# Optimization experiments

Hardware: AMD Instinct MI355X
Metric: run time of the kernel (lower is better)

Reference implementation:

```python
import jax, jax.numpy as jnp
import numpy as np

N, E = 50000, 800000
F_IN, HID, H, LBL = 512, 16, 8, 40
HC = HID * H  # 128
BN_EPS = 1e-5
ELU_ALPHA = 0.2
NEG_SLOPE = 0.2


def setup_inputs() -> dict:
    key = jax.random.key(0)
    ks = jax.random.split(key, 32)
    inp = {}
    inp['x'] = jax.random.normal(ks[0], (N, F_IN), dtype=jnp.float32)
    inp['edge_index'] = jax.random.randint(ks[1], (2, E), 0, N, dtype=jnp.int32)
    # layer 0: F_IN -> (H, HID), concat
    inp['W0'] = jax.random.normal(ks[2], (F_IN, HC), dtype=jnp.float32) * 0.05
    inp['as0'] = jax.random.normal(ks[3], (H, HID), dtype=jnp.float32) * 0.1
    inp['ad0'] = jax.random.normal(ks[4], (H, HID), dtype=jnp.float32) * 0.1
    inp['b0'] = jnp.zeros((HC,), jnp.float32)
    inp['g0'] = jnp.ones((HC,), jnp.float32)
    inp['be0'] = jnp.zeros((HC,), jnp.float32)
    inp['rm0'] = jnp.zeros((HC,), jnp.float32)
    inp['rv0'] = jnp.ones((HC,), jnp.float32)
    # layer 1: HC -> (H, HID), concat
    inp['W1'] = jax.random.normal(ks[5], (HC, HC), dtype=jnp.float32) * 0.1
    inp['as1'] = jax.random.normal(ks[6], (H, HID), dtype=jnp.float32) * 0.1
    inp['ad1'] = jax.random.normal(ks[7], (H, HID), dtype=jnp.float32) * 0.1
    inp['b1'] = jnp.zeros((HC,), jnp.float32)
    inp['g1'] = jnp.ones((HC,), jnp.float32)
    inp['be1'] = jnp.zeros((HC,), jnp.float32)
    inp['rm1'] = jnp.zeros((HC,), jnp.float32)
    inp['rv1'] = jnp.ones((HC,), jnp.float32)
    # layer 2: HC -> (1, LBL), mean (concat=False)
    inp['W2'] = jax.random.normal(ks[8], (HC, LBL), dtype=jnp.float32) * 0.1
    inp['as2'] = jax.random.normal(ks[9], (1, LBL), dtype=jnp.float32) * 0.1
    inp['ad2'] = jax.random.normal(ks[10], (1, LBL), dtype=jnp.float32) * 0.1
    inp['b2'] = jnp.zeros((LBL,), jnp.float32)
    return inp


def _gat_conv(xf, src, dst, W, a_src, a_dst, b, heads, out_ch, concat):
    # PyG GATConv (eval): linear -> per-head attn logits -> segment softmax over dst -> scatter-add
    n = xf.shape[0]
    h = (xf @ W).reshape(n, heads, out_ch)            # [N,H,C]
    alpha_s = jnp.einsum('nhc,hc->nh', h, a_src)      # [N,H]
    alpha_d = jnp.einsum('nhc,hc->nh', h, a_dst)
    e = jax.nn.leaky_relu(alpha_s[src] + alpha_d[dst], NEG_SLOPE)  # [Etot,H]
    m = jax.ops.segment_max(e, dst, num_segments=n)
    e = jnp.exp(e - m[dst])
    s = jax.ops.segment_sum(e, dst, num_segments=n)
    alpha = e / (s[dst] + 1e-16)                      # [Etot,H]
    msg = alpha[:, :, None] * h[src]                  # [Etot,H,C]
    out = jax.ops.segment_sum(msg, dst, num_segments=n)  # [N,H,C]
    out = out.reshape(n, heads * out_ch) if concat else out.mean(axis=1)
    return out + b


def _bn_elu(xf, g, be, rm, rv):
    y = (xf - rm) * (g * jax.lax.rsqrt(rv + BN_EPS)) + be
    return jnp.where(y > 0, y, ELU_ALPHA * jnp.expm1(y))


def reference(x, edge_index, W0, as0, ad0, b0, g0, be0, rm0, rv0,
              W1, as1, ad1, b1, g1, be1, rm1, rv1, W2, as2, ad2, b2):
    n = x.shape[0]
    # add self-loops (PyG GATConv default add_self_loops=True)
    loops = jnp.arange(n, dtype=edge_index.dtype)
    src = jnp.concatenate([edge_index[0], loops])
    dst = jnp.concatenate([edge_index[1], loops])
    h = _gat_conv(x, src, dst, W0, as0, ad0, b0, H, HID, True)
    h = _bn_elu(h, g0, be0, rm0, rv0)
    h = _gat_conv(h, src, dst, W1, as1, ad1, b1, H, HID, True)
    h = _bn_elu(h, g1, be1, rm1, rv1)
    out = _gat_conv(h, src, dst, W2, as2, ad2, b2, 1, LBL, False)
    return out
```

## Files before the change

### kernel.cpp

```cpp
#include <hip/hip_runtime.h>
#include <hip/hip_bf16.h>
#include <cstdint>
#include <cstddef>

#define NN 50000
#define EE 800000
#define FIN 512
#define HIDC 16
#define NH 8
#define HCH 128
#define NLBL 40
#define NLBLP 48
#define ETOT (EE + NN)
#define NEG_SLOPE 0.2f
#define ELU_A 0.2f
#define BN_EPS 1e-5f
#define SCH 8192
#define NCHK 7

typedef __attribute__((ext_vector_type(8))) short bf16x8;
typedef __attribute__((ext_vector_type(4))) short bf16x4;
typedef __attribute__((ext_vector_type(4))) float f32x4;

__device__ inline short f2b(float f) {
    __hip_bfloat16 h = __float2bfloat16(f);
    return *reinterpret_cast<short*>(&h);
}
__device__ inline float blo(unsigned int u) {
    union { unsigned int u; float f; } v; v.u = u << 16; return v.f;
}
__device__ inline float bhi(unsigned int u) {
    union { unsigned int u; float f; } v; v.u = u & 0xffff0000u; return v.f;
}

__global__ __launch_bounds__(256) void k_prep(const float* __restrict__ W0, short* __restrict__ Wt0,
                                              const float* __restrict__ W1, short* __restrict__ Wt1,
                                              const float* __restrict__ W2, short* __restrict__ Wt2,
                                              const int* __restrict__ ei, int* __restrict__ deg)
{
    int b = blockIdx.x;
    int tid = threadIdx.x;
    if (b < 256) {
        int idx = b * 256 + tid;
        int n = idx >> 9, k = idx & 511;
        Wt0[idx] = f2b(W0[(size_t)k * HCH + n]);
        return;
    }
    b -= 256;
    if (b < 64) {
        int idx = b * 256 + tid;
        int n = idx >> 7, k = idx & 127;
        Wt1[idx] = f2b(W1[(size_t)k * HCH + n]);
        return;
    }
    b -= 64;
    if (b < 24) {
        int idx = b * 256 + tid;
        int n = idx >> 7, k = idx & 127;
        Wt2[idx] = f2b(n < NLBL ? W2[(size_t)k * NLBL + n] : 0.f);
        return;
    }
    b -= 24;
    {
        int e = b * 256 + tid;
        if (e < ETOT) {
            int dst = (e < EE) ? ei[EE + e] : (e - EE);
            atomicAdd(&deg[dst], 1);
        }
    }
}

__global__ __launch_bounds__(1024) void k_scan1(const int* __restrict__ deg,
                                                int* __restrict__ row_ptr,
                                                int* __restrict__ tot)
{
    __shared__ int sm[1024];
    int b = blockIdx.x, tid = threadIdx.x;
    int i0 = b * SCH + tid * 8;
    int v[8];
    int s = 0;
    #pragma unroll
    for (int j = 0; j < 8; ++j) {
        int i = i0 + j;
        v[j] = (i < NN) ? deg[i] : 0;
        s += v[j];
    }
    sm[tid] = s;
    __syncthreads();
    for (int ofs = 1; ofs < 1024; ofs <<= 1) {
        int t = (tid >= ofs) ? sm[tid - ofs] : 0;
        __syncthreads();
        sm[tid] += t;
        __syncthreads();
    }
    int excl = sm[tid] - s;
    #pragma unroll
    for (int j = 0; j < 8; ++j) {
        int i = i0 + j;
        if (i < NN) row_ptr[i] = excl;
        excl += v[j];
    }
    if (tid == 1023) tot[b] = sm[1023];
}

__global__ __launch_bounds__(64) void k_scan2(const int* __restrict__ tot,
                                              int* __restrict__ totp,
                                              int* __restrict__ row_ptr)
{
    if (threadIdx.x == 0) {
        int run = 0;
        for (int i = 0; i < NCHK; ++i) { totp[i] = run; run += tot[i]; }
        row_ptr[NN] = run;
    }
}

__global__ __launch_bounds__(256) void k_scan3(int* __restrict__ row_ptr,
                                               int* __restrict__ cursor,
                                               const int* __restrict__ totp)
{
    int i = blockIdx.x * 256 + threadIdx.x;
    if (i < NN) {
        int v = row_ptr[i] + totp[i / SCH];
        row_ptr[i] = v;
        cursor[i] = v;
    }
}

__global__ __launch_bounds__(256) void k_scatter(const int* __restrict__ ei,
                                                 int* __restrict__ cursor,
                                                 int* __restrict__ csr_src)
{
    int e = blockIdx.x * blockDim.x + threadIdx.x;
    if (e >= ETOT) return;
    int src, dst;
    if (e < EE) { src = ei[e]; dst = ei[EE + e]; }
    else        { src = dst = e - EE; }
    int pos = atomicAdd(&cursor[dst], 1);
    csr_src[pos] = src;
}

template<int KDIM, bool A_BF16>
__global__ __launch_bounds__(512, 4) void k_gemm2(const void* __restrict__ Ap,
                                                  const short* __restrict__ Wt,
                                                  short* __restrict__ C,
                                                  int M,
                                                  const float* __restrict__ a_s,
                                                  const float* __restrict__ a_d,
                                                  float* __restrict__ as_o,
                                                  float* __restrict__ ad_o)
{
    constexpr int KCH  = 128;
    constexpr int NCH  = KDIM / KCH;
    constexpr int LROW = KCH + 8;
    __shared__ short As[64 * LROW];
    __shared__ short Bs[128 * LROW];

    const int tid  = threadIdx.x;
    const int wv   = tid >> 6;
    const int lane = tid & 63;
    const int quad = lane >> 4;
    const int col  = lane & 15;
    const int wr   = wv >> 1;
    const int wn   = wv & 1;
    const int rowbase = blockIdx.x * 64;

    const float* Af = (const float*)Ap;
    const short* Ab = (const short*)Ap;

    float4 pa[4];
    bf16x8 pab[2];
    bf16x8 pb[4];

    auto loadA = [&](int c) {
        if constexpr (A_BF16) {
            #pragma unroll
            for (int r = 0; r < 2; ++r) {
                int gr = rowbase + r * 32 + (tid >> 4);
                gr = gr < M ? gr : M - 1;
                pab[r] = *(const bf16x8*)(Ab + (size_t)gr * KDIM + c * KCH + (tid & 15) * 8);
            }
        } else {
            #pragma unroll
            for (int r = 0; r < 4; ++r) {
                int gr = rowbase + r * 16 + (tid >> 5);
                gr = gr < M ? gr : M - 1;
                pa[r] = *(const float4*)(Af + (size_t)gr * KDIM + c * KCH + (tid & 31) * 4);
            }
        }
    };
    auto loadB = [&](int c) {
        #pragma unroll
        for (int r = 0; r < 4; ++r) {
            int n = r * 32 + (tid >> 4);
            pb[r] = *(const bf16x8*)(Wt + (size_t)n * KDIM + c * KCH + (tid & 15) * 8);
        }
    };
    auto writeAB = [&]() {
        if constexpr (A_BF16) {
            #pragma unroll
            for (int r = 0; r < 2; ++r) {
                int row = r * 32 + (tid >> 4);
                *(bf16x8*)(As + row * LROW + (tid & 15) * 8) = pab[r];
            }
        } else {
            #pragma unroll
            for (int r = 0; r < 4; ++r) {
                int row = r * 16 + (tid >> 5);
                bf16x4 w;
                w[0] = f2b(pa[r].x); w[1] = f2b(pa[r].y);
                w[2] = f2b(pa[r].z); w[3] = f2b(pa[r].w);
                *(bf16x4*)(As + row * LROW + (tid & 31) * 4) = w;
            }
        }
        #pragma unroll
        for (int r = 0; r < 4; ++r) {
            int n = r * 32 + (tid >> 4);
            *(bf16x8*)(Bs + n * LROW + (tid & 15) * 8) = pb[r];
        }
    };

    f32x4 acc[4];
    #pragma unroll
    for (int t = 0; t < 4; ++t) acc[t] = (f32x4){0.f, 0.f, 0.f, 0.f};

    loadA(0); loadB(0);

    for (int c = 0; c < NCH; ++c) {
        writeAB();
        __syncthreads();
        if (c + 1 < NCH) { loadA(c + 1); loadB(c + 1); }
        #pragma unroll
        for (int s = 0; s < KCH / 32; ++s) {
            bf16x8 af = *(const bf16x8*)(As + (wr * 16 + col) * LROW + s * 32 + quad * 8);
            #pragma unroll
            for (int t = 0; t < 4; ++t) {
                bf16x8 bf = *(const bf16x8*)(Bs + (wn * 64 + t * 16 + col) * LROW + s * 32 + quad * 8);
                acc[t] = __builtin_amdgcn_mfma_f32_16x16x32_bf16(af, bf, acc[t], 0, 0, 0);
            }
        }
        if (c + 1 < NCH) __syncthreads();
    }

    const int mb = rowbase + wr * 16 + quad * 4;

    #pragma unroll
    for (int t = 0; t < 4; ++t) {
        int cc = wn * 64 + t * 16 + col;
        #pragma unroll
        for (int r = 0; r < 4; ++r) {
            int m = mb + r;
            if (m < M) C[(size_t)m * HCH + cc] = f2b(acc[t][r]);
        }
    }

    #pragma unroll
    for (int t = 0; t < 4; ++t) {
        int hh = wn * 4 + t;
        float ws = a_s[hh * HIDC + col];
        float wd = a_d[hh * HIDC + col];
        #pragma unroll
        for (int r = 0; r < 4; ++r) {
            float vs = acc[t][r] * ws;
            float vd = acc[t][r] * wd;
            vs += __shfl_xor(vs, 1);  vd += __shfl_xor(vd, 1);
            vs += __shfl_xor(vs, 2);  vd += __shfl_xor(vd, 2);
            vs += __shfl_xor(vs, 4);  vd += __shfl_xor(vd, 4);
            vs += __shfl_xor(vs, 8);  vd += __shfl_xor(vd, 8);
            int m = mb + r;
            if (col == 0 && m < M) {
                as_o[m * NH + hh] = vs;
                ad_o[m * NH + hh] = vd;
            }
        }
    }
}

template<int KDIM, int NTILES, bool A_BF16>
__global__ __launch_bounds__(256) void k_gemm_lds(const void* __restrict__ Ap,
                                                  const short* __restrict__ Wt,
                                                  short* __restrict__ C,
                                                  int M, int N,
                                                  const float* __restrict__ a_s2,
                                                  const float* __restrict__ a_d2,
                                                  float* __restrict__ as_o,
                                                  float* __restrict__ ad_o)
{
    constexpr int NFULL = NTILES * 16;
    constexpr int KCH = 128;
    constexpr int NK = KDIM / 32;
    constexpr int NCH = KDIM / KCH;
    constexpr int LROW = KCH + 8;
    __shared__ short Bs[NFULL * LROW];

    const int tid  = threadIdx.x;
    const int wave = tid >> 6;
    const int lane = tid & 63;
    const int quad = lane >> 4;
    const int col  = lane & 15;
    const int row  = blockIdx.x * 64 + wave * 16 + col;
    const int arow = row < M ? row : M - 1;

    f32x4 acc[NTILES];
    #pragma unroll
    for (int t = 0; t < NTILES; ++t) acc[t] = (f32x4){0.f, 0.f, 0.f, 0.f};

    bf16x8 arB[4];
    float4 arF[4][2];
    const short* Ab = (const short*)Ap;
    const float* Af = (const float*)Ap;
    auto pf = [&](int ks) {
        if (ks >= NK) return;
        if (A_BF16) {
            arB[ks & 3] = *(const bf16x8*)(Ab + (size_t)arow * KDIM + ks * 32 + quad * 8);
        } else {
            const float4* p = (const float4*)(Af + (size_t)arow * KDIM + ks * 32 + quad * 8);
            arF[ks & 3][0] = p[0];
            arF[ks & 3][1] = p[1];
        }
    };
    pf(0); pf(1); pf(2); pf(3);

    for (int c = 0; c < NCH; ++c) {
        const int k0 = c * KCH;
        constexpr int TOT8 = NFULL * (KCH / 8);
        #pragma unroll
        for (int i = tid; i < TOT8; i += 256) {
            int n  = i >> 4;
            int kk = i & 15;
            bf16x8 v = *(const bf16x8*)(Wt + (size_t)n * KDIM + k0 + kk * 8);
            *(bf16x8*)(Bs + n * LROW + kk * 8) = v;
        }
        __syncthreads();
        #pragma unroll
        for (int s = 0; s < KCH / 32; ++s) {
            const int ks = c * (KCH / 32) + s;
            bf16x8 afrag;
            if (A_BF16) {
                afrag = arB[ks & 3];
            } else {
                float4 v0 = arF[ks & 3][0], v1 = arF[ks & 3][1];
                afrag[0] = f2b(v0.x); afrag[1] = f2b(v0.y);
                afrag[2] = f2b(v0.z); afrag[3] = f2b(v0.w);
                afrag[4] = f2b(v1.x); afrag[5] = f2b(v1.y);
                afrag[6] = f2b(v1.z); afrag[7] = f2b(v1.w);
            }
            pf(ks + 4);
            #pragma unroll
            for (int t = 0; t < NTILES; ++t) {
                bf16x8 bfrag = *(const bf16x8*)(Bs + (t * 16 + col) * LROW + s * 32 + quad * 8);
                acc[t] = __builtin_amdgcn_mfma_f32_16x16x32_bf16(afrag, bfrag, acc[t], 0, 0, 0);
            }
        }
        if (c + 1 < NCH) __syncthreads();
    }

    const int mbase = blockIdx.x * 64 + wave * 16 + quad * 4;
    #pragma unroll
    for (int t = 0; t < NTILES; ++t) {
        int cc = t * 16 + col;
        if (cc < N) {
            #pragma unroll
            for (int r = 0; r < 4; ++r) {
                int m = mbase + r;
                if (m < M) C[(size_t)m * N + cc] = f2b(acc[t][r]);
            }
        }
    }

    float vs[4] = {0.f, 0.f, 0.f, 0.f};
    float vd[4] = {0.f, 0.f, 0.f, 0.f};
    #pragma unroll
    for (int t = 0; t < NTILES; ++t) {
        int cc = t * 16 + col;
        float ws = cc < NLBL ? a_s2[cc] : 0.f;
        float wd = cc < NLBL ? a_d2[cc] : 0.f;
        #pragma unroll
        for (int r = 0; r < 4; ++r) {
            vs[r] += acc[t][r] * ws;
            vd[r] += acc[t][r] * wd;
        }
    }
    #pragma unroll
    for (int r = 0; r < 4; ++r) {
        float s = vs[r], d = vd[r];
        s += __shfl_xor(s, 1);  d += __shfl_xor(d, 1);
        s += __shfl_xor(s, 2);  d += __shfl_xor(d, 2);
        s += __shfl_xor(s, 4);  d += __shfl_xor(d, 4);
        s += __shfl_xor(s, 8);  d += __shfl_xor(d, 8);
        int m = mbase + r;
        if (col == 0 && m < M) {
            as_o[m] = s;
            ad_o[m] = d;
        }
    }
}

__global__ __launch_bounds__(256) void k_agg(const int* __restrict__ row_ptr,
                                             const int* __restrict__ csr_src,
                                             const unsigned short* __restrict__ h,
                                             const float* __restrict__ as,
                                             const float* __restrict__ ad,
                                             const float* __restrict__ b,
                                             const float* __restrict__ g,
                                             const float* __restrict__ be,
                                             const float* __restrict__ rm,
                                             const float* __restrict__ rv,
                                             short* __restrict__ out)
{
    int n = blockIdx.x * 4 + (threadIdx.x >> 6);
    if (n >= NN) return;
    int lane = threadIdx.x & 63;
    int half = lane >> 5;
    int c4 = lane & 31;
    int hh = c4 >> 2;
    float adv = ad[n * NH + hh];
    float a0 = 0.f, a1 = 0.f, a2 = 0.f, a3 = 0.f, sw = 0.f;
    int jb = row_ptr[n], je = row_ptr[n + 1];
    int j = jb + half;
    for (; j + 6 < je; j += 8) {
        int s0 = csr_src[j];
        int s1 = csr_src[j + 2];
        int s2 = csr_src[j + 4];
        int s3 = csr_src[j + 6];
        float l0 = as[s0 * NH + hh] + adv;
        float l1 = as[s1 * NH + hh] + adv;
        float l2 = as[s2 * NH + hh] + adv;
        float l3 = as[s3 * NH + hh] + adv;
        uint2 u0 = *(const uint2*)(h + (size_t)s0 * HCH + 4 * c4);
        uint2 u1 = *(const uint2*)(h + (size_t)s1 * HCH + 4 * c4);
        uint2 u2 = *(const uint2*)(h + (size_t)s2 * HCH + 4 * c4);
        uint2 u3 = *(const uint2*)(h + (size_t)s3 * HCH + 4 * c4);
        l0 = l0 > 0.f ? l0 : NEG_SLOPE * l0;
        l1 = l1 > 0.f ? l1 : NEG_SLOPE * l1;
        l2 = l2 > 0.f ? l2 : NEG_SLOPE * l2;
        l3 = l3 > 0.f ? l3 : NEG_SLOPE * l3;
        float w0 = __expf(l0), w1 = __expf(l1), w2 = __expf(l2), w3 = __expf(l3);
        sw += (w0 + w1) + (w2 + w3);
        a0 += w0 * blo(u0.x) + w1 * blo(u1.x) + w2 * blo(u2.x) + w3 * blo(u3.x);
        a1 += w0 * bhi(u0.x) + w1 * bhi(u1.x) + w2 * bhi(u2.x) + w3 * bhi(u3.x);
        a2 += w0 * blo(u0.y) + w1 * blo(u1.y) + w2 * blo(u2.y) + w3 * blo(u3.y);
        a3 += w0 * bhi(u0.y) + w1 * bhi(u1.y) + w2 * bhi(u2.y) + w3 * bhi(u3.y);
    }
    for (; j < je; j += 2) {
        int s0 = csr_src[j];
        float l0 = as[s0 * NH + hh] + adv;
        uint2 u0 = *(const uint2*)(h + (size_t)s0 * HCH + 4 * c4);
        l0 = l0 > 0.f ? l0 : NEG_SLOPE * l0;
        float w0 = __expf(l0);
        sw += w0;
        a0 += w0 * blo(u0.x);
        a1 += w0 * bhi(u0.x);
        a2 += w0 * blo(u0.y);
        a3 += w0 * bhi(u0.y);
    }
    a0 += __shfl_down(a0, 32);
    a1 += __shfl_down(a1, 32);
    a2 += __shfl_down(a2, 32);
    a3 += __shfl_down(a3, 32);
    sw += __shfl_down(sw, 32);
    if (half == 0) {
        int c = 4 * c4;
        float inv = 1.f / (sw + 1e-16f);
        float4 bv  = *(const float4*)(b + c);
        float4 gv  = *(const float4*)(g + c);
        float4 bev = *(const float4*)(be + c);
        float4 rmv = *(const float4*)(rm + c);
        float4 rvv = *(const float4*)(rv + c);
        float r0 = a0 * inv + bv.x;
        float r1 = a1 * inv + bv.y;
        float r2 = a2 * inv + bv.z;
        float r3 = a3 * inv + bv.w;
        r0 = (r0 - rmv.x) * (gv.x * rsqrtf(rvv.x + BN_EPS)) + bev.x;
        r1 = (r1 - rmv.y) * (gv.y * rsqrtf(rvv.y + BN_EPS)) + bev.y;
        r2 = (r2 - rmv.z) * (gv.z * rsqrtf(rvv.z + BN_EPS)) + bev.z;
        r3 = (r3 - rmv.w) * (gv.w * rsqrtf(rvv.w + BN_EPS)) + bev.w;
        r0 = r0 > 0.f ? r0 : ELU_A * expm1f(r0);
        r1 = r1 > 0.f ? r1 : ELU_A * expm1f(r1);
        r2 = r2 > 0.f ? r2 : ELU_A * expm1f(r2);
        r3 = r3 > 0.f ? r3 : ELU_A * expm1f(r3);
        unsigned int lo = (unsigned int)(unsigned short)f2b(r0) |
                          ((unsigned int)(unsigned short)f2b(r1) << 16);
        unsigned int hi = (unsigned int)(unsigned short)f2b(r2) |
                          ((unsigned int)(unsigned short)f2b(r3) << 16);
        *(uint2*)(out + (size_t)n * HCH + c) = make_uint2(lo, hi);
    }
}

__global__ __launch_bounds__(256) void k_agg2(const int* __restrict__ row_ptr,
                                              const int* __restrict__ csr_src,
                                              const unsigned short* __restrict__ h2,
                                              const float* __restrict__ as,
                                              const float* __restrict__ ad,
                                              const float* __restrict__ b,
                                              float* __restrict__ out)
{
    int n = blockIdx.x * 4 + (threadIdx.x >> 6);
    if (n >= NN) return;
    int lane = threadIdx.x & 63;
    int half = lane >> 5;
    int c2 = lane & 31;
    bool act = c2 < 20;
    int coff = act ? 2 * c2 : 0;
    float adv = ad[n];
    float acc0 = 0.f, acc1 = 0.f, sw = 0.f;
    int jb = row_ptr[n], je = row_ptr[n + 1];
    int j = jb + half;
    for (; j + 6 < je; j += 8) {
        int s0 = csr_src[j];
        int s1 = csr_src[j + 2];
        int s2 = csr_src[j + 4];
        int s3 = csr_src[j + 6];
        float l0 = as[s0] + adv;
        float l1 = as[s1] + adv;
        float l2 = as[s2] + adv;
        float l3 = as[s3] + adv;
        unsigned int u0 = *(const unsigned int*)(h2 + (size_t)s0 * NLBL + coff);
        unsigned int u1 = *(const unsigned int*)(h2 + (size_t)s1 * NLBL + coff);
        unsigned int u2 = *(const unsigned int*)(h2 + (size_t)s2 * NLBL + coff);
        unsigned int u3 = *(const unsigned int*)(h2 + (size_t)s3 * NLBL + coff);
        l0 = l0 > 0.f ? l0 : NEG_SLOPE * l0;
        l1 = l1 > 0.f ? l1 : NEG_SLOPE * l1;
        l2 = l2 > 0.f ? l2 : NEG_SLOPE * l2;
        l3 = l3 > 0.f ? l3 : NEG_SLOPE * l3;
        float w0 = __expf(l0), w1 = __expf(l1), w2 = __expf(l2), w3 = __expf(l3);
        sw += (w0 + w1) + (w2 + w3);
        if (act) {
            acc0 += w0 * blo(u0) + w1 * blo(u1) + w2 * blo(u2) + w3 * blo(u3);
            acc1 += w0 * bhi(u0) + w1 * bhi(u1) + w2 * bhi(u2) + w3 * bhi(u3);
        }
    }
    for (; j < je; j += 2) {
        int s = csr_src[j];
        float l = as[s] + adv;
        unsigned int u = *(const unsigned int*)(h2 + (size_t)s * NLBL + coff);
        l = l > 0.f ? l : NEG_SLOPE * l;
        float w = __expf(l);
        sw += w;
        if (act) {
            acc0 += w * blo(u);
            acc1 += w * bhi(u);
        }
    }
    float acc0b = __shfl_down(acc0, 32);
    float acc1b = __shfl_down(acc1, 32);
    float swb   = __shfl_down(sw, 32);
    if (half == 0 && act) {
        acc0 += acc0b; acc1 += acc1b; sw += swb;
        float inv = 1.f / (sw + 1e-16f);
        out[(size_t)n * NLBL + 2 * c2]     = acc0 * inv + b[2 * c2];
        out[(size_t)n * NLBL + 2 * c2 + 1] = acc1 * inv + b[2 * c2 + 1];
    }
}

extern "C" void kernel_launch(void* const* d_in, const int* in_sizes, int n_in,
                              void* d_out, int out_size, void* d_ws, size_t ws_size,
                              hipStream_t stream)
{
    const float* x   = (const float*)d_in[0];
    const int*   ei  = (const int*)d_in[1];
    const float* W0  = (const float*)d_in[2];
    const float* as0 = (const float*)d_in[3];
    const float* ad0 = (const float*)d_in[4];
    const float* b0  = (const float*)d_in[5];
    const float* g0  = (const float*)d_in[6];
    const float* be0 = (const float*)d_in[7];
    const float* rm0 = (const float*)d_in[8];
    const float* rv0 = (const float*)d_in[9];
    const float* W1  = (const float*)d_in[10];
    const float* as1 = (const float*)d_in[11];
    const float* ad1 = (const float*)d_in[12];
    const float* b1  = (const float*)d_in[13];
    const float* g1  = (const float*)d_in[14];
    const float* be1 = (const float*)d_in[15];
    const float* rm1 = (const float*)d_in[16];
    const float* rv1 = (const float*)d_in[17];
    const float* W2  = (const float*)d_in[18];
    const float* a_s2 = (const float*)d_in[19];
    const float* a_d2 = (const float*)d_in[20];
    const float* b2  = (const float*)d_in[21];
    float* out = (float*)d_out;

    char* ws = (char*)d_ws;
    size_t off = 0;
    auto alloc = [&](size_t bytes) {
        void* p = (void*)(ws + off);
        off += (bytes + 255) & ~(size_t)255;
        return p;
    };
    short* hbuf   = (short*)alloc((size_t)NN * HCH * 2);
    short* fbuf   = (short*)alloc((size_t)NN * HCH * 2);
    float* asb    = (float*)alloc((size_t)NN * NH * 4);
    float* adb    = (float*)alloc((size_t)NN * NH * 4);
    int*   deg    = (int*)alloc((size_t)NN * 4);
    int*   rowp   = (int*)alloc((size_t)(NN + 1) * 4);
    int*   cursor = (int*)alloc((size_t)NN * 4);
    int*   csrs   = (int*)alloc((size_t)ETOT * 4);
    short* Wt0    = (short*)alloc((size_t)HCH * FIN * 2);
    short* Wt1    = (short*)alloc((size_t)HCH * HCH * 2);
    short* Wt2    = (short*)alloc((size_t)NLBLP * HCH * 2);
    int*   tot    = (int*)alloc(64 * 4);
    int*   totp   = (int*)alloc(64 * 4);
    short* h2     = hbuf;

    const int T = 256;
    const int gN4 = (NN + 3) / 4;
    const int gM  = (NN + 63) / 64;
    const int gPrep = 256 + 64 + 24 + (ETOT + T - 1) / T;
    const int gE  = (ETOT + T - 1) / T;

    hipMemsetAsync(deg, 0, (size_t)NN * 4, stream);
    k_prep<<<gPrep, T, 0, stream>>>(W0, Wt0, W1, Wt1, W2, Wt2, ei, deg);

    k_scan1<<<NCHK, 1024, 0, stream>>>(deg, rowp, tot);
    k_scan2<<<1, 64, 0, stream>>>(tot, totp, rowp);
    k_scan3<<<(NN + T - 1) / T, T, 0, stream>>>(rowp, cursor, totp);
    k_scatter<<<gE, T, 0, stream>>>(ei, cursor, csrs);

    k_gemm2<FIN, false><<<gM, 512, 0, stream>>>(x, Wt0, hbuf, NN, as0, ad0, asb, adb);
    k_agg<<<gN4, T, 0, stream>>>(rowp, csrs, (const unsigned short*)hbuf, asb, adb,
                                 b0, g0, be0, rm0, rv0, fbuf);

    k_gemm2<HCH, true><<<gM, 512, 0, stream>>>(fbuf, Wt1, hbuf, NN, as1, ad1, asb, adb);
    k_agg<<<gN4, T, 0, stream>>>(rowp, csrs, (const unsigned short*)hbuf, asb, adb,
                                 b1, g1, be1, rm1, rv1, fbuf);

    k_gemm_lds<HCH, 3, true><<<gM, T, 0, stream>>>(fbuf, Wt2, h2, NN, NLBL,
                                                   a_s2, a_d2, asb, adb);
    k_agg2<<<gN4, T, 0, stream>>>(rowp, csrs, (const unsigned short*)h2, asb, adb, b2, out);
}
```

Baseline: 455.5 us.

## Double-buffer GEMM K-chunks and unroll gather loops to eight edges

The GEMM now uses K-chunks of 64 and two register prefetch buffers, so global loads for chunk c+2 are issued while chunk c is being computed, which deepens latency hiding. The aggregation kernels for the hidden and output layers get a 16-edge main loop with 8 independent gathers in flight per thread, to raise memory-level parallelism on the random neighbour reads. The costs are more registers and possible occupancy loss, plus twice as many syncthreads per K in the GEMM.

```diff
diff --git a/kernel.cpp b/kernel.cpp
--- a/kernel.cpp
+++ b/kernel.cpp
@@ -149,7 +149,7 @@
                                                   float* __restrict__ as_o,
                                                   float* __restrict__ ad_o)
 {
-    constexpr int KCH  = 128;
+    constexpr int KCH  = 64;
     constexpr int NCH  = KDIM / KCH;
     constexpr int LROW = KCH + 8;
     __shared__ short As[64 * LROW];
@@ -167,55 +167,49 @@
     const float* Af = (const float*)Ap;
     const short* Ab = (const short*)Ap;
 
-    float4 pa[4];
-    bf16x8 pab[2];
-    bf16x8 pb[4];
-
-    auto loadA = [&](int c) {
+    float4 paA[2], paB[2];
+    bf16x8 pabA, pabB;
+    bf16x8 pbA[2], pbB[2];
+
+    auto loadA = [&](int c, float4* pa, bf16x8& pab) {
         if constexpr (A_BF16) {
+            int gr = rowbase + (tid >> 3);
+            gr = gr < M ? gr : M - 1;
+            pab = *(const bf16x8*)(Ab + (size_t)gr * KDIM + c * KCH + (tid & 7) * 8);
+        } else {
             #pragma unroll
             for (int r = 0; r < 2; ++r) {
                 int gr = rowbase + r * 32 + (tid >> 4);
                 gr = gr < M ? gr : M - 1;
-                pab[r] = *(const bf16x8*)(Ab + (size_t)gr * KDIM + c * KCH + (tid & 15) * 8);
-            }
+                pa[r] = *(const float4*)(Af + (size_t)gr * KDIM + c * KCH + (tid & 15) * 4);
+            }
+        }
+    };
+    auto loadB = [&](int c, bf16x8* pb) {
+        #pragma unroll
+        for (int r = 0; r < 2; ++r) {
+            int n = r * 64 + (tid >> 3);
+            pb[r] = *(const bf16x8*)(Wt + (size_t)n * KDIM + c * KCH + (tid & 7) * 8);
+        }
+    };
+    auto writeAB = [&](const float4* pa, const bf16x8& pab, const bf16x8* pb) {
+        if constexpr (A_BF16) {
+            int row = tid >> 3;
+            *(bf16x8*)(As + row * LROW + (tid & 7) * 8) = pab;
         } else {
-            #pragma unroll
-            for (int r = 0; r < 4; ++r) {
-                int gr = rowbase + r * 16 + (tid >> 5);
-                gr = gr < M ? gr : M - 1;
-                pa[r] = *(const float4*)(Af + (size_t)gr * KDIM + c * KCH + (tid & 31) * 4);
-            }
-        }
-    };
-    auto loadB = [&](int c) {
-        #pragma unroll
-        for (int r = 0; r < 4; ++r) {
-            int n = r * 32 + (tid >> 4);
-            pb[r] = *(const bf16x8*)(Wt + (size_t)n * KDIM + c * KCH + (tid & 15) * 8);
-        }
-    };
-    auto writeAB = [&]() {
-        if constexpr (A_BF16) {
             #pragma unroll
             for (int r = 0; r < 2; ++r) {
                 int row = r * 32 + (tid >> 4);
-                *(bf16x8*)(As + row * LROW + (tid & 15) * 8) = pab[r];
-            }
-        } else {
-            #pragma unroll
-            for (int r = 0; r < 4; ++r) {
-                int row = r * 16 + (tid >> 5);
                 bf16x4 w;
                 w[0] = f2b(pa[r].x); w[1] = f2b(pa[r].y);
                 w[2] = f2b(pa[r].z); w[3] = f2b(pa[r].w);
-                *(bf16x4*)(As + row * LROW + (tid & 31) * 4) = w;
-            }
-        }
-        #pragma unroll
-        for (int r = 0; r < 4; ++r) {
-            int n = r * 32 + (tid >> 4);
-            *(bf16x8*)(Bs + n * LROW + (tid & 15) * 8) = pb[r];
+                *(bf16x4*)(As + row * LROW + (tid & 15) * 4) = w;
+            }
+        }
+        #pragma unroll
+        for (int r = 0; r < 2; ++r) {
+            int n = r * 64 + (tid >> 3);
+            *(bf16x8*)(Bs + n * LROW + (tid & 7) * 8) = pb[r];
         }
     };
 
@@ -223,12 +217,18 @@
     #pragma unroll
     for (int t = 0; t < 4; ++t) acc[t] = (f32x4){0.f, 0.f, 0.f, 0.f};
 
-    loadA(0); loadB(0);
-
+    loadA(0, paA, pabA); loadB(0, pbA);
+    if constexpr (NCH > 1) { loadA(1, paB, pabB); loadB(1, pbB); }
+
+    #pragma unroll
     for (int c = 0; c < NCH; ++c) {
-        writeAB();
+        if (c & 1) writeAB(paB, pabB, pbB);
+        else       writeAB(paA, pabA, pbA);
         __syncthreads();
-        if (c + 1 < NCH) { loadA(c + 1); loadB(c + 1); }
+        if (c + 2 < NCH) {
+            if (c & 1) { loadA(c + 2, paB, pabB); loadB(c + 2, pbB); }
+            else       { loadA(c + 2, paA, pabA); loadB(c + 2, pbA); }
+        }
         #pragma unroll
         for (int s = 0; s < KCH / 32; ++s) {
             bf16x8 af = *(const bf16x8*)(As + (wr * 16 + col) * LROW + s * 32 + quad * 8);
@@ -417,6 +417,28 @@
     float a0 = 0.f, a1 = 0.f, a2 = 0.f, a3 = 0.f, sw = 0.f;
     int jb = row_ptr[n], je = row_ptr[n + 1];
     int j = jb + half;
+    for (; j + 14 < je; j += 16) {
+        int s[8];
+        #pragma unroll
+        for (int q = 0; q < 8; ++q) s[q] = csr_src[j + 2 * q];
+        float l[8];
+        uint2 u[8];
+        #pragma unroll
+        for (int q = 0; q < 8; ++q) {
+            l[q] = as[s[q] * NH + hh] + adv;
+            u[q] = *(const uint2*)(h + (size_t)s[q] * HCH + 4 * c4);
+        }
+        #pragma unroll
+        for (int q = 0; q < 8; ++q) {
+            float lq = l[q] > 0.f ? l[q] : NEG_SLOPE * l[q];
+            float w = __expf(lq);
+            sw += w;
+            a0 += w * blo(u[q].x);
+            a1 += w * bhi(u[q].x);
+            a2 += w * blo(u[q].y);
+            a3 += w * bhi(u[q].y);
+        }
+    }
     for (; j + 6 < je; j += 8) {
         int s0 = csr_src[j];
         int s1 = csr_src[j + 2];
@@ -505,6 +527,28 @@
     float acc0 = 0.f, acc1 = 0.f, sw = 0.f;
     int jb = row_ptr[n], je = row_ptr[n + 1];
     int j = jb + half;
+    for (; j + 14 < je; j += 16) {
+        int s[8];
+        #pragma unroll
+        for (int q = 0; q < 8; ++q) s[q] = csr_src[j + 2 * q];
+        float l[8];
+        unsigned int u[8];
+        #pragma unroll
+        for (int q = 0; q < 8; ++q) {
+            l[q] = as[s[q]] + adv;
+            u[q] = *(const unsigned int*)(h2 + (size_t)s[q] * NLBL + coff);
+        }
+        #pragma unroll
+        for (int q = 0; q < 8; ++q) {
+            float lq = l[q] > 0.f ? l[q] : NEG_SLOPE * l[q];
+            float w = __expf(lq);
+            sw += w;
+            if (act) {
+                acc0 += w * blo(u[q]);
+                acc1 += w * bhi(u[q]);
+            }
+        }
+    }
     for (; j + 6 < je; j += 8) {
         int s0 = csr_src[j];
         int s1 = csr_src[j + 2];
```

Measured after the change: 460.7 us. No clear change (+1.1%).
